# Kernel tuning notes

Hardware: AMD Instinct MI355X
Metric: run time of the kernel (lower is better)

Reference implementation:

```python
import jax, jax.numpy as jnp
import numpy as np

N_NODES = 100000
N_EDGES = 1600000
HIDDEN = 128
NUM_FILTERS = 128
NUM_GAUSSIANS = 50
CUTOFF = 10.0
BOX = 5.0  # positions in [0,5]^3 so all pairwise distances < cutoff


def shifted_softplus(x):
    return jax.nn.softplus(x) - jnp.log(2.0)


def setup_inputs() -> dict:
    key = jax.random.key(0)
    ks = jax.random.split(key, 12)
    h = jax.random.normal(ks[0], (N_NODES, HIDDEN), jnp.float32)
    pos = jax.random.uniform(ks[1], (N_NODES, 3), jnp.float32) * BOX
    edge_index = jax.random.randint(ks[2], (2, N_EDGES), 0, N_NODES, jnp.int32)
    def lin(k, fan_in, fan_out):
        s = 1.0 / np.sqrt(fan_in)
        return jax.random.uniform(k, (fan_in, fan_out), jnp.float32, -s, s)
    return {
        "h": h,
        "pos": pos,
        "edge_index": edge_index,
        # CFConv filter network: Linear(NG, NF) -> ssp -> Linear(NF, NF)
        "mlp_w1": lin(ks[3], NUM_GAUSSIANS, NUM_FILTERS),
        "mlp_b1": jnp.zeros((NUM_FILTERS,), jnp.float32),
        "mlp_w2": lin(ks[4], NUM_FILTERS, NUM_FILTERS),
        "mlp_b2": jnp.zeros((NUM_FILTERS,), jnp.float32),
        # CFConv lin1 (no bias), lin2
        "lin1_w": lin(ks[5], HIDDEN, NUM_FILTERS),
        "lin2_w": lin(ks[6], NUM_FILTERS, HIDDEN),
        "lin2_b": jnp.zeros((HIDDEN,), jnp.float32),
        # InteractionBlock output linear
        "lin_w": lin(ks[7], HIDDEN, HIDDEN),
        "lin_b": jnp.zeros((HIDDEN,), jnp.float32),
    }


def reference(h, pos, edge_index, mlp_w1, mlp_b1, mlp_w2, mlp_b2,
              lin1_w, lin2_w, lin2_b, lin_w, lin_b):
    row, col = edge_index[0], edge_index[1]
    # edge distances (radius_graph neighbor list precomputed in setup_inputs)
    d = jnp.linalg.norm(pos[row] - pos[col], axis=-1)  # [E]
    # Gaussian smearing
    offset = jnp.linspace(0.0, CUTOFF, NUM_GAUSSIANS)
    coeff = -0.5 / (offset[1] - offset[0]) ** 2
    edge_attr = jnp.exp(coeff * (d[:, None] - offset[None, :]) ** 2)  # [E, NG]
    # CFConv: cosine cutoff * filter MLP
    C = 0.5 * (jnp.cos(d * jnp.pi / CUTOFF) + 1.0)  # [E]
    W = shifted_softplus(edge_attr @ mlp_w1 + mlp_b1) @ mlp_w2 + mlp_b2
    W = W * C[:, None]  # [E, NF]
    x = h @ lin1_w  # [N, NF]
    msgs = x[col] * W  # gather source feats, modulate by filter
    agg = jax.ops.segment_sum(msgs, row, num_segments=h.shape[0])  # scatter-add
    x = agg @ lin2_w + lin2_b
    # InteractionBlock tail: act -> linear
    x = shifted_softplus(x)
    x = x @ lin_w + lin_b
    return x
```

## Files before the change

### kernel.cpp

```cpp
#include <hip/hip_runtime.h>
#include <hip/hip_fp16.h>
#include <math.h>

constexpr int N_NODES = 100000;
constexpr int N_EDGES = 1600000;
constexpr int H       = 128;
constexpr int NG      = 50;
constexpr int EPT     = 32;
constexpr int NT      = N_EDGES / EPT;
constexpr int EBLK    = 2560;
constexpr int NBINS   = 98 * 1024;
constexpr int NODEB   = N_NODES / 32;

typedef _Float16 f16x8 __attribute__((ext_vector_type(8)));
typedef float    f32x4 __attribute__((ext_vector_type(4)));

__device__ __forceinline__ float ssp_fast(float v) {
    return fmaxf(v, 0.0f) + __logf(1.0f + __expf(-fabsf(v))) - 0.69314718056f;
}

__device__ __forceinline__ void stage_tile_fp16(
    const float* __restrict__ src, _Float16* lds, int tid)
{
    const int row = tid >> 3;
    const int c0  = (tid & 7) * 16;
    const float* s = src + row * H + c0;
    #pragma unroll
    for (int half = 0; half < 2; ++half) {
        float4 f0 = *reinterpret_cast<const float4*>(s + half * 8);
        float4 f1 = *reinterpret_cast<const float4*>(s + half * 8 + 4);
        f16x8 v;
        v[0] = (_Float16)f0.x; v[1] = (_Float16)f0.y;
        v[2] = (_Float16)f0.z; v[3] = (_Float16)f0.w;
        v[4] = (_Float16)f1.x; v[5] = (_Float16)f1.y;
        v[6] = (_Float16)f1.z; v[7] = (_Float16)f1.w;
        unsigned off = (unsigned)(row * H + c0 + half * 8) * 2u;
        off ^= (unsigned)((row & 7) << 4);
        *reinterpret_cast<f16x8*>(reinterpret_cast<char*>(lds) + off) = v;
    }
}

__global__ __launch_bounds__(256) void prep0_kernel(
    const float* __restrict__ h, const float* __restrict__ w,
    __half* __restrict__ x, int* __restrict__ bins, float* __restrict__ agg)
{
    __shared__ alignas(16) _Float16 a_lds[32 * H];

    const int tid  = threadIdx.x;
    const int gtid = blockIdx.x * 256 + tid;
    const int gsz  = NODEB * 256;

    for (int i = gtid; i < NBINS; i += gsz) bins[i] = 0;
    {
        float4 z = {0.0f, 0.0f, 0.0f, 0.0f};
        float4* agg4 = reinterpret_cast<float4*>(agg);
        for (int i = gtid; i < N_NODES * H / 4; i += gsz) agg4[i] = z;
    }

    const int wv  = tid >> 6;
    const int l   = tid & 63;
    const int lhi = l >> 4;
    const int llo = l & 15;

    f16x8 bf[2][4];
    #pragma unroll
    for (int nf = 0; nf < 2; ++nf) {
        const int n = wv * 32 + nf * 16 + llo;
        #pragma unroll
        for (int ks = 0; ks < 4; ++ks)
            #pragma unroll
            for (int i = 0; i < 8; ++i)
                bf[nf][ks][i] = (_Float16)w[(ks * 32 + lhi * 8 + i) * H + n];
    }

    stage_tile_fp16(h + (size_t)blockIdx.x * 32 * H, a_lds, tid);
    __syncthreads();

    const f32x4 zero4 = {0.0f, 0.0f, 0.0f, 0.0f};
    f32x4 c[2][2];
    #pragma unroll
    for (int m = 0; m < 2; ++m)
        #pragma unroll
        for (int nf = 0; nf < 2; ++nf) c[m][nf] = zero4;

    #pragma unroll
    for (int msub = 0; msub < 2; ++msub) {
        const int rowa = msub * 16 + llo;
        #pragma unroll
        for (int ks = 0; ks < 4; ++ks) {
            unsigned off = (unsigned)(rowa * H) * 2u + (unsigned)(ks * 64 + lhi * 16);
            off ^= (unsigned)((rowa & 7) << 4);
            const f16x8 a = *reinterpret_cast<const f16x8*>(
                reinterpret_cast<const char*>(a_lds) + off);
            #pragma unroll
            for (int nf = 0; nf < 2; ++nf)
                c[msub][nf] = __builtin_amdgcn_mfma_f32_16x16x32_f16(
                    a, bf[nf][ks], c[msub][nf], 0, 0, 0);
        }
    }

    #pragma unroll
    for (int msub = 0; msub < 2; ++msub)
        #pragma unroll
        for (int nf = 0; nf < 2; ++nf)
            #pragma unroll
            for (int j = 0; j < 4; ++j) {
                const int node = blockIdx.x * 32 + msub * 16 + lhi * 4 + j;
                const int filt = wv * 32 + nf * 16 + llo;
                x[(size_t)node * H + filt] = __float2half(c[msub][nf][j]);
            }
}

__global__ __launch_bounds__(256) void hist_kernel(
    const int* __restrict__ ei, int* __restrict__ bins)
{
    const int e = blockIdx.x * 256 + threadIdx.x;
    if (e < N_EDGES) atomicAdd(&bins[ei[e]], 1);
}

__global__ __launch_bounds__(1024) void scanA_kernel(
    int* __restrict__ bins, int* __restrict__ bsum)
{
    __shared__ int ts[1024];
    const int i = blockIdx.x * 1024 + threadIdx.x;
    const int v = bins[i];
    ts[threadIdx.x] = v;
    __syncthreads();
    for (int d = 1; d < 1024; d <<= 1) {
        int t = (threadIdx.x >= d) ? ts[threadIdx.x - d] : 0;
        __syncthreads();
        ts[threadIdx.x] += t;
        __syncthreads();
    }
    bins[i] = ts[threadIdx.x] - v;
    if (threadIdx.x == 1023) bsum[blockIdx.x] = ts[1023];
}

__global__ __launch_bounds__(128) void scanB_kernel(int* __restrict__ bsum)
{
    __shared__ int ts[128];
    const int i = threadIdx.x;
    const int v = (i < 98) ? bsum[i] : 0;
    ts[i] = v;
    __syncthreads();
    for (int d = 1; d < 128; d <<= 1) {
        int t = (i >= d) ? ts[i - d] : 0;
        __syncthreads();
        ts[i] += t;
        __syncthreads();
    }
    if (i < 98) bsum[i] = ts[i] - v;
}

__global__ __launch_bounds__(256) void scatter_kernel(
    const int* __restrict__ ei, int* __restrict__ bins,
    const int* __restrict__ bsum, int2* __restrict__ srt)
{
    const int e = blockIdx.x * 256 + threadIdx.x;
    if (e < N_EDGES) {
        const int r = ei[e];
        const int c = ei[N_EDGES + e];
        const int p = atomicAdd(&bins[r], 1) + bsum[r >> 10];
        srt[p] = make_int2(r, c);
    }
}

__global__ __launch_bounds__(256) void edge_kernel(
    const float* __restrict__ pos, const int2* __restrict__ srt,
    const __half* __restrict__ x,
    const float* __restrict__ w1, const float* __restrict__ b1,
    const float* __restrict__ w2, const float* __restrict__ b2,
    float* __restrict__ agg)
{
    __shared__ alignas(16) _Float16 t_lds[EPT * H];
    __shared__ alignas(16) _Float16 attr_lds[EPT * 64];

    const int tid = threadIdx.x;
    const int w   = tid >> 6;
    const int l   = tid & 63;
    const int lhi = l >> 4;
    const int llo = l & 15;

    constexpr float GSTEP = 10.0f / 49.0f;
    constexpr float GCOEF = -12.005f;
    constexpr float PIC   = 0.31415926535897931f;

    f16x8 b1f[2][2];
    #pragma unroll
    for (int nf = 0; nf < 2; ++nf) {
        const int n = w * 32 + nf * 16 + llo;
        #pragma unroll
        for (int ks = 0; ks < 2; ++ks) {
            #pragma unroll
            for (int i = 0; i < 8; ++i) {
                const int k = ks * 32 + lhi * 8 + i;
                b1f[nf][ks][i] = (k < NG) ? (_Float16)w1[k * H + n] : (_Float16)0.0f;
            }
        }
    }
    f16x8 b2f[2][4];
    #pragma unroll
    for (int nf = 0; nf < 2; ++nf) {
        const int n = w * 32 + nf * 16 + llo;
        #pragma unroll
        for (int ks = 0; ks < 4; ++ks) {
            #pragma unroll
            for (int i = 0; i < 8; ++i) {
                const int k = ks * 32 + lhi * 8 + i;
                b2f[nf][ks][i] = (_Float16)w2[k * H + n];
            }
        }
    }
    const float b1v[2] = { b1[w * 32 + llo], b1[w * 32 + 16 + llo] };
    const float b2v[2] = { b2[w * 32 + llo], b2[w * 32 + 16 + llo] };

    const f32x4 zero4 = {0.0f, 0.0f, 0.0f, 0.0f};

    int rC = 0, cC = 0; float dC = 0.0f, ccC = 0.0f;
    auto load_edge = [&](int t, int& r, int& c, float& d, float& cc) {
        const int2 rc = srt[t * EPT + (l & 31)];
        r = rc.x;
        c = rc.y;
        const float dx = pos[3 * r + 0] - pos[3 * c + 0];
        const float dy = pos[3 * r + 1] - pos[3 * c + 1];
        const float dz = pos[3 * r + 2] - pos[3 * c + 2];
        d  = sqrtf(dx * dx + dy * dy + dz * dz);
        cc = 0.5f * cosf(d * PIC) + 0.5f;
    };
    if (l < 32) load_edge(blockIdx.x, rC, cC, dC, ccC);

    for (int t = blockIdx.x; t < NT; t += gridDim.x) {
        {
            const int ae = w * 8 + (l >> 3);
            const int g0 = (l & 7) * 8;
            const float de = __shfl(dC, ae);
            f16x8 av;
            #pragma unroll
            for (int i = 0; i < 8; ++i) {
                const float diff = de - (float)(g0 + i) * GSTEP;
                av[i] = (_Float16)__expf(GCOEF * diff * diff);
            }
            unsigned off = (unsigned)(ae * 128 + (l & 7) * 16);
            off ^= (unsigned)((ae & 7) << 4);
            *reinterpret_cast<f16x8*>(
                reinterpret_cast<char*>(attr_lds) + off) = av;
        }

        int rN = 0, cN = 0; float dN = 0.0f, ccN = 0.0f;
        const int tn = t + gridDim.x;
        if (l < 32 && tn < NT) load_edge(tn, rN, cN, dN, ccN);

        __syncthreads();

        float xv[2][4][2];
        #pragma unroll
        for (int msub = 0; msub < 2; ++msub)
            #pragma unroll
            for (int j = 0; j < 4; ++j) {
                const int edge  = msub * 16 + lhi * 4 + j;
                const int ce    = __shfl(cC, edge);
                const int cbase = ce * H + w * 32 + llo;
                xv[msub][j][0] = __half2float(x[cbase]);
                xv[msub][j][1] = __half2float(x[cbase + 16]);
            }

        f32x4 c1[2][2];
        #pragma unroll
        for (int m = 0; m < 2; ++m)
            #pragma unroll
            for (int nf = 0; nf < 2; ++nf) c1[m][nf] = zero4;

        #pragma unroll
        for (int msub = 0; msub < 2; ++msub) {
            const int ea = msub * 16 + llo;
            #pragma unroll
            for (int ks = 0; ks < 2; ++ks) {
                unsigned off = (unsigned)(ea * 128 + ks * 64 + lhi * 16);
                off ^= (unsigned)((ea & 7) << 4);
                const f16x8 a1 = *reinterpret_cast<const f16x8*>(
                    reinterpret_cast<const char*>(attr_lds) + off);
                #pragma unroll
                for (int nf = 0; nf < 2; ++nf)
                    c1[msub][nf] = __builtin_amdgcn_mfma_f32_16x16x32_f16(
                        a1, b1f[nf][ks], c1[msub][nf], 0, 0, 0);
            }
        }

        #pragma unroll
        for (int msub = 0; msub < 2; ++msub)
            #pragma unroll
            for (int nf = 0; nf < 2; ++nf)
                #pragma unroll
                for (int j = 0; j < 4; ++j) {
                    const int edge = msub * 16 + lhi * 4 + j;
                    const int filt = w * 32 + nf * 16 + llo;
                    const float tv = ssp_fast(c1[msub][nf][j] + b1v[nf]);
                    unsigned off = (unsigned)(edge * H + filt) * 2u;
                    off ^= (unsigned)((edge & 7) << 4);
                    *reinterpret_cast<_Float16*>(
                        reinterpret_cast<char*>(t_lds) + off) = (_Float16)tv;
                }

        __syncthreads();

        f32x4 c2[2][2];
        #pragma unroll
        for (int m = 0; m < 2; ++m)
            #pragma unroll
            for (int nf = 0; nf < 2; ++nf) c2[m][nf] = zero4;

        #pragma unroll
        for (int ks = 0; ks < 4; ++ks) {
            f16x8 a2[2];
            #pragma unroll
            for (int msub = 0; msub < 2; ++msub) {
                const int edge = msub * 16 + llo;
                unsigned off = (unsigned)(edge * H) * 2u
                             + (unsigned)(ks * 64 + lhi * 16);
                off ^= (unsigned)((edge & 7) << 4);
                a2[msub] = *reinterpret_cast<const f16x8*>(
                    reinterpret_cast<const char*>(t_lds) + off);
            }
            #pragma unroll
            for (int msub = 0; msub < 2; ++msub)
                #pragma unroll
                for (int nf = 0; nf < 2; ++nf)
                    c2[msub][nf] = __builtin_amdgcn_mfma_f32_16x16x32_f16(
                        a2[msub], b2f[nf][ks], c2[msub][nf], 0, 0, 0);
        }

        #pragma unroll
        for (int msub = 0; msub < 2; ++msub) {
            int rr[4]; float cce[4];
            #pragma unroll
            for (int j = 0; j < 4; ++j) {
                const int edge = msub * 16 + lhi * 4 + j;
                rr[j]  = __shfl(rC, edge);
                cce[j] = __shfl(ccC, edge);
            }
            const bool bB1 = rr[1] != rr[0];
            const bool bB2 = rr[2] != rr[1];
            const bool bB3 = rr[3] != rr[2];
            const bool closed = bB1 | bB2 | bB3;
            const int  prev_t = __shfl_up(rr[3], 16);
            const int  next_h = __shfl_down(rr[0], 16);
            const bool mrg  = (lhi > 0) && (rr[0] == prev_t);
            const bool sing = !closed;
            const bool issue_tail = (lhi == 3) || (next_h != rr[3]);

            float v0[4], v1[4];
            #pragma unroll
            for (int j = 0; j < 4; ++j) {
                v0[j] = (c2[msub][0][j] + b2v[0]) * cce[j] * xv[msub][j][0];
                v1[j] = (c2[msub][1][j] + b2v[1]) * cce[j] * xv[msub][j][1];
            }
            const int fc0 = w * 32 + llo;
            const int fc1 = fc0 + 16;

            float h0 = v0[0], h1 = v1[0];
            if (!bB1) { h0 += v0[1]; h1 += v1[1];
                if (!bB2) { h0 += v0[2]; h1 += v1[2];
                    if (!bB3) { h0 += v0[3]; h1 += v1[3]; } } }
            float cs0 = v0[3], cs1 = v1[3];
            if (!bB3) { cs0 += v0[2]; cs1 += v1[2];
                if (!bB2) { cs0 += v0[1]; cs1 += v1[1];
                    if (!bB1) { cs0 += v0[0]; cs1 += v1[0]; } } }

            if (bB1 && bB2) { atomicAdd(&agg[rr[1] * H + fc0], v0[1]);
                              atomicAdd(&agg[rr[1] * H + fc1], v1[1]); }
            if (bB2 && bB3) { atomicAdd(&agg[rr[2] * H + fc0], v0[2]);
                              atomicAdd(&agg[rr[2] * H + fc1], v1[2]); }
            if (bB1 && !bB2 && bB3) {
                atomicAdd(&agg[rr[1] * H + fc0], v0[1] + v0[2]);
                atomicAdd(&agg[rr[1] * H + fc1], v1[1] + v1[2]);
            }

            bool f = !(sing && mrg);
            {
                float p0 = __shfl_up(cs0, 16), p1 = __shfl_up(cs1, 16);
                int   pf = __shfl_up((int)f, 16);
                if (lhi >= 1 && !f) { cs0 += p0; cs1 += p1; f = (bool)pf; }
            }
            {
                float p0 = __shfl_up(cs0, 32), p1 = __shfl_up(cs1, 32);
                int   pf = __shfl_up((int)f, 32);
                if (lhi >= 2 && !f) { cs0 += p0; cs1 += p1; f = (bool)pf; }
            }
            const float car0 = __shfl_up(cs0, 16);
            const float car1 = __shfl_up(cs1, 16);

            if (closed) {
                atomicAdd(&agg[rr[0] * H + fc0], h0 + (mrg ? car0 : 0.0f));
                atomicAdd(&agg[rr[0] * H + fc1], h1 + (mrg ? car1 : 0.0f));
            }
            if (issue_tail) {
                atomicAdd(&agg[rr[3] * H + fc0], cs0);
                atomicAdd(&agg[rr[3] * H + fc1], cs1);
            }
        }

        rC = rN; cC = cN; dC = dN; ccC = ccN;
    }
}

__global__ __launch_bounds__(256) void final_kernel(
    const float* __restrict__ agg,
    const float* __restrict__ w2l, const float* __restrict__ b2l,
    const float* __restrict__ wl,  const float* __restrict__ bl,
    float* __restrict__ out)
{
    __shared__ alignas(16) _Float16 a_lds[32 * H];
    __shared__ alignas(16) _Float16 t_lds[32 * H];

    const int tid = threadIdx.x;
    const int wv  = tid >> 6;
    const int l   = tid & 63;
    const int lhi = l >> 4;
    const int llo = l & 15;

    f16x8 b1f[2][4], b2f[2][4];
    #pragma unroll
    for (int nf = 0; nf < 2; ++nf) {
        const int n = wv * 32 + nf * 16 + llo;
        #pragma unroll
        for (int ks = 0; ks < 4; ++ks)
            #pragma unroll
            for (int i = 0; i < 8; ++i) {
                const int k = ks * 32 + lhi * 8 + i;
                b1f[nf][ks][i] = (_Float16)w2l[k * H + n];
                b2f[nf][ks][i] = (_Float16)wl[k * H + n];
            }
    }
    const float b2v[2] = { b2l[wv * 32 + llo], b2l[wv * 32 + 16 + llo] };
    const float bv[2]  = { bl[wv * 32 + llo],  bl[wv * 32 + 16 + llo]  };

    stage_tile_fp16(agg + (size_t)blockIdx.x * 32 * H, a_lds, tid);
    __syncthreads();

    const f32x4 zero4 = {0.0f, 0.0f, 0.0f, 0.0f};
    f32x4 c1[2][2];
    #pragma unroll
    for (int m = 0; m < 2; ++m)
        #pragma unroll
        for (int nf = 0; nf < 2; ++nf) c1[m][nf] = zero4;

    #pragma unroll
    for (int msub = 0; msub < 2; ++msub) {
        const int rowa = msub * 16 + llo;
        #pragma unroll
        for (int ks = 0; ks < 4; ++ks) {
            unsigned off = (unsigned)(rowa * H) * 2u + (unsigned)(ks * 64 + lhi * 16);
            off ^= (unsigned)((rowa & 7) << 4);
            const f16x8 a = *reinterpret_cast<const f16x8*>(
                reinterpret_cast<const char*>(a_lds) + off);
            #pragma unroll
            for (int nf = 0; nf < 2; ++nf)
                c1[msub][nf] = __builtin_amdgcn_mfma_f32_16x16x32_f16(
                    a, b1f[nf][ks], c1[msub][nf], 0, 0, 0);
        }
    }

    #pragma unroll
    for (int msub = 0; msub < 2; ++msub)
        #pragma unroll
        for (int nf = 0; nf < 2; ++nf)
            #pragma unroll
            for (int j = 0; j < 4; ++j) {
                const int rowc = msub * 16 + lhi * 4 + j;
                const int filt = wv * 32 + nf * 16 + llo;
                const float tv = ssp_fast(c1[msub][nf][j] + b2v[nf]);
                unsigned off = (unsigned)(rowc * H + filt) * 2u;
                off ^= (unsigned)((rowc & 7) << 4);
                *reinterpret_cast<_Float16*>(
                    reinterpret_cast<char*>(t_lds) + off) = (_Float16)tv;
            }

    __syncthreads();

    f32x4 c2[2][2];
    #pragma unroll
    for (int m = 0; m < 2; ++m)
        #pragma unroll
        for (int nf = 0; nf < 2; ++nf) c2[m][nf] = zero4;

    #pragma unroll
    for (int msub = 0; msub < 2; ++msub) {
        const int rowa = msub * 16 + llo;
        #pragma unroll
        for (int ks = 0; ks < 4; ++ks) {
            unsigned off = (unsigned)(rowa * H) * 2u + (unsigned)(ks * 64 + lhi * 16);
            off ^= (unsigned)((rowa & 7) << 4);
            const f16x8 a = *reinterpret_cast<const f16x8*>(
                reinterpret_cast<const char*>(t_lds) + off);
            #pragma unroll
            for (int nf = 0; nf < 2; ++nf)
                c2[msub][nf] = __builtin_amdgcn_mfma_f32_16x16x32_f16(
                    a, b2f[nf][ks], c2[msub][nf], 0, 0, 0);
        }
    }

    #pragma unroll
    for (int msub = 0; msub < 2; ++msub)
        #pragma unroll
        for (int nf = 0; nf < 2; ++nf)
            #pragma unroll
            for (int j = 0; j < 4; ++j) {
                const int node = blockIdx.x * 32 + msub * 16 + lhi * 4 + j;
                const int filt = wv * 32 + nf * 16 + llo;
                out[(size_t)node * H + filt] = c2[msub][nf][j] + bv[nf];
            }
}

extern "C" void kernel_launch(void* const* d_in, const int* in_sizes, int n_in,
                              void* d_out, int out_size, void* d_ws, size_t ws_size,
                              hipStream_t stream) {
    const float* h      = (const float*)d_in[0];
    const float* pos    = (const float*)d_in[1];
    const int*   ei     = (const int*)  d_in[2];
    const float* mlp_w1 = (const float*)d_in[3];
    const float* mlp_b1 = (const float*)d_in[4];
    const float* mlp_w2 = (const float*)d_in[5];
    const float* mlp_b2 = (const float*)d_in[6];
    const float* lin1_w = (const float*)d_in[7];
    const float* lin2_w = (const float*)d_in[8];
    const float* lin2_b = (const float*)d_in[9];
    const float* lin_w  = (const float*)d_in[10];
    const float* lin_b  = (const float*)d_in[11];

    float* out = (float*)d_out;
    char*  ws  = (char*)d_ws;
    float* agg  = (float*)ws;
    char*  p    = ws + (size_t)N_NODES * H * 4;
    int*   bins = (int*)p;
    int*   bsum = (int*)(p + (size_t)NBINS * 4);
    int2*  srt  = (int2*)(p + (size_t)NBINS * 4 + 512);
    __half* x   = (__half*)d_out;

    prep0_kernel<<<NODEB, 256, 0, stream>>>(h, lin1_w, x, bins, agg);
    hist_kernel<<<(N_EDGES + 255) / 256, 256, 0, stream>>>(ei, bins);
    scanA_kernel<<<NBINS / 1024, 1024, 0, stream>>>(bins, bsum);
    scanB_kernel<<<1, 128, 0, stream>>>(bsum);
    scatter_kernel<<<(N_EDGES + 255) / 256, 256, 0, stream>>>(ei, bins, bsum, srt);

    edge_kernel<<<EBLK, 256, 0, stream>>>(pos, srt, x, mlp_w1, mlp_b1,
                                          mlp_w2, mlp_b2, agg);
    final_kernel<<<NODEB, 256, 0, stream>>>(agg, lin2_w, lin2_b,
                                            lin_w, lin_b, out);
}
```

Before: 576.8 us.

## Precompute edge distance and cutoff in scatter; sparse Gaussian smearing in edge kernel

The small bsum scan is folded into every scatter block, which removes one launch. Edge distance and cosine cutoff are now computed in the scatter pass and stored with the sorted (row, col) as an int4 record. The edge kernel then reads this record directly instead of gathering pos and shuffling across lanes. Gaussian smearing now evaluates only a 16-wide window of Gaussians around each distance and zero-fills the rest. This cuts exp work, at the cost of an extra LDS clear plus barrier per tile and a small approximation from the truncated tails. The sorted metadata doubles in size and is stored in the output buffer's spare space.

```diff
diff --git a/kernel.cpp b/kernel.cpp
--- a/kernel.cpp
+++ b/kernel.cpp
@@ -13,6 +13,7 @@
 constexpr int NODEB   = N_NODES / 32;
 
 typedef _Float16 f16x8 __attribute__((ext_vector_type(8)));
+typedef _Float16 f16x2 __attribute__((ext_vector_type(2)));
 typedef float    f32x4 __attribute__((ext_vector_type(4)));
 
 __device__ __forceinline__ float ssp_fast(float v) {
@@ -136,38 +137,44 @@
     if (threadIdx.x == 1023) bsum[blockIdx.x] = ts[1023];
 }
 
-__global__ __launch_bounds__(128) void scanB_kernel(int* __restrict__ bsum)
-{
-    __shared__ int ts[128];
-    const int i = threadIdx.x;
-    const int v = (i < 98) ? bsum[i] : 0;
-    ts[i] = v;
+__global__ __launch_bounds__(256) void scatter_kernel(
+    const int* __restrict__ ei, const float* __restrict__ pos,
+    int* __restrict__ bins, const int* __restrict__ bsum,
+    int4* __restrict__ meta)
+{
+    __shared__ int pre[128];
+    const int tid = threadIdx.x;
+    int myv = 0;
+    if (tid < 128) {
+        myv = (tid < 98) ? bsum[tid] : 0;
+        pre[tid] = myv;
+    }
     __syncthreads();
     for (int d = 1; d < 128; d <<= 1) {
-        int t = (i >= d) ? ts[i - d] : 0;
-        __syncthreads();
-        ts[i] += t;
-        __syncthreads();
-    }
-    if (i < 98) bsum[i] = ts[i] - v;
-}
-
-__global__ __launch_bounds__(256) void scatter_kernel(
-    const int* __restrict__ ei, int* __restrict__ bins,
-    const int* __restrict__ bsum, int2* __restrict__ srt)
-{
-    const int e = blockIdx.x * 256 + threadIdx.x;
+        int t = (tid < 128 && tid >= d) ? pre[tid - d] : 0;
+        __syncthreads();
+        if (tid < 128) pre[tid] += t;
+        __syncthreads();
+    }
+    if (tid < 128) pre[tid] -= myv;
+    __syncthreads();
+
+    const int e = blockIdx.x * 256 + tid;
     if (e < N_EDGES) {
         const int r = ei[e];
         const int c = ei[N_EDGES + e];
-        const int p = atomicAdd(&bins[r], 1) + bsum[r >> 10];
-        srt[p] = make_int2(r, c);
+        const int p = atomicAdd(&bins[r], 1) + pre[r >> 10];
+        const float dx = pos[3 * r + 0] - pos[3 * c + 0];
+        const float dy = pos[3 * r + 1] - pos[3 * c + 1];
+        const float dz = pos[3 * r + 2] - pos[3 * c + 2];
+        const float d  = sqrtf(dx * dx + dy * dy + dz * dz);
+        const float cc = 0.5f * cosf(d * 0.31415926535897931f) + 0.5f;
+        meta[p] = make_int4(r, __float_as_int(cc), c, __float_as_int(d));
     }
 }
 
 __global__ __launch_bounds__(256) void edge_kernel(
-    const float* __restrict__ pos, const int2* __restrict__ srt,
-    const __half* __restrict__ x,
+    const int4* __restrict__ meta, const __half* __restrict__ x,
     const float* __restrict__ w1, const float* __restrict__ b1,
     const float* __restrict__ w2, const float* __restrict__ b2,
     float* __restrict__ agg)
@@ -182,8 +189,8 @@
     const int llo = l & 15;
 
     constexpr float GSTEP = 10.0f / 49.0f;
+    constexpr float GINV  = 4.9f;
     constexpr float GCOEF = -12.005f;
-    constexpr float PIC   = 0.31415926535897931f;
 
     f16x8 b1f[2][2];
     #pragma unroll
@@ -215,41 +222,35 @@
     const float b2v[2] = { b2[w * 32 + llo], b2[w * 32 + 16 + llo] };
 
     const f32x4 zero4 = {0.0f, 0.0f, 0.0f, 0.0f};
-
-    int rC = 0, cC = 0; float dC = 0.0f, ccC = 0.0f;
-    auto load_edge = [&](int t, int& r, int& c, float& d, float& cc) {
-        const int2 rc = srt[t * EPT + (l & 31)];
-        r = rc.x;
-        c = rc.y;
-        const float dx = pos[3 * r + 0] - pos[3 * c + 0];
-        const float dy = pos[3 * r + 1] - pos[3 * c + 1];
-        const float dz = pos[3 * r + 2] - pos[3 * c + 2];
-        d  = sqrtf(dx * dx + dy * dy + dz * dz);
-        cc = 0.5f * cosf(d * PIC) + 0.5f;
-    };
-    if (l < 32) load_edge(blockIdx.x, rC, cC, dC, ccC);
+    const f16x8 zf16  = {(_Float16)0, (_Float16)0, (_Float16)0, (_Float16)0,
+                         (_Float16)0, (_Float16)0, (_Float16)0, (_Float16)0};
 
     for (int t = blockIdx.x; t < NT; t += gridDim.x) {
+        const int4* mt = meta + (size_t)t * EPT;
+
+        *reinterpret_cast<f16x8*>(
+            reinterpret_cast<char*>(attr_lds) + tid * 16) = zf16;
+        __syncthreads();
+
         {
-            const int ae = w * 8 + (l >> 3);
-            const int g0 = (l & 7) * 8;
-            const float de = __shfl(dC, ae);
-            f16x8 av;
-            #pragma unroll
-            for (int i = 0; i < 8; ++i) {
-                const float diff = de - (float)(g0 + i) * GSTEP;
-                av[i] = (_Float16)__expf(GCOEF * diff * diff);
-            }
-            unsigned off = (unsigned)(ae * 128 + (l & 7) * 16);
+            const int ae = tid >> 3;
+            const int p  = tid & 7;
+            const float d = __int_as_float(
+                reinterpret_cast<const int*>(mt + ae)[3]);
+            int g0 = (int)(d * GINV + 0.5f) - 7;
+            g0 &= ~1;
+            g0 = max(0, min(48, g0));
+            const int g = g0 + 2 * p;
+            const float df0 = d - (float)g * GSTEP;
+            const float df1 = d - (float)(g + 1) * GSTEP;
+            f16x2 v;
+            v[0] = (_Float16)__expf(GCOEF * df0 * df0);
+            v[1] = (_Float16)__expf(GCOEF * df1 * df1);
+            unsigned off = (unsigned)(ae * 128 + g * 2);
             off ^= (unsigned)((ae & 7) << 4);
-            *reinterpret_cast<f16x8*>(
-                reinterpret_cast<char*>(attr_lds) + off) = av;
-        }
-
-        int rN = 0, cN = 0; float dN = 0.0f, ccN = 0.0f;
-        const int tn = t + gridDim.x;
-        if (l < 32 && tn < NT) load_edge(tn, rN, cN, dN, ccN);
-
+            *reinterpret_cast<f16x2*>(
+                reinterpret_cast<char*>(attr_lds) + off) = v;
+        }
         __syncthreads();
 
         float xv[2][4][2];
@@ -257,9 +258,9 @@
         for (int msub = 0; msub < 2; ++msub)
             #pragma unroll
             for (int j = 0; j < 4; ++j) {
-                const int edge  = msub * 16 + lhi * 4 + j;
-                const int ce    = __shfl(cC, edge);
-                const int cbase = ce * H + w * 32 + llo;
+                const int edge = msub * 16 + lhi * 4 + j;
+                const int col  = reinterpret_cast<const int*>(mt + edge)[2];
+                const int cbase = col * H + w * 32 + llo;
                 xv[msub][j][0] = __half2float(x[cbase]);
                 xv[msub][j][1] = __half2float(x[cbase + 16]);
             }
@@ -303,6 +304,14 @@
 
         __syncthreads();
 
+        int2 rcA[2][4];
+        #pragma unroll
+        for (int msub = 0; msub < 2; ++msub)
+            #pragma unroll
+            for (int j = 0; j < 4; ++j)
+                rcA[msub][j] = *reinterpret_cast<const int2*>(
+                    mt + msub * 16 + lhi * 4 + j);
+
         f32x4 c2[2][2];
         #pragma unroll
         for (int m = 0; m < 2; ++m)
@@ -334,9 +343,8 @@
             int rr[4]; float cce[4];
             #pragma unroll
             for (int j = 0; j < 4; ++j) {
-                const int edge = msub * 16 + lhi * 4 + j;
-                rr[j]  = __shfl(rC, edge);
-                cce[j] = __shfl(ccC, edge);
+                rr[j]  = rcA[msub][j].x;
+                cce[j] = __int_as_float(rcA[msub][j].y);
             }
             const bool bB1 = rr[1] != rr[0];
             const bool bB2 = rr[2] != rr[1];
@@ -398,8 +406,6 @@
                 atomicAdd(&agg[rr[3] * H + fc1], cs1);
             }
         }
-
-        rC = rN; cC = cN; dC = dN; ccC = ccN;
     }
 }
 
@@ -533,16 +539,16 @@
     char*  p    = ws + (size_t)N_NODES * H * 4;
     int*   bins = (int*)p;
     int*   bsum = (int*)(p + (size_t)NBINS * 4);
-    int2*  srt  = (int2*)(p + (size_t)NBINS * 4 + 512);
-    __half* x   = (__half*)d_out;
+
+    __half* x    = (__half*)d_out;
+    int4*   meta = (int4*)((char*)d_out + (size_t)N_NODES * H * 2);
 
     prep0_kernel<<<NODEB, 256, 0, stream>>>(h, lin1_w, x, bins, agg);
     hist_kernel<<<(N_EDGES + 255) / 256, 256, 0, stream>>>(ei, bins);
     scanA_kernel<<<NBINS / 1024, 1024, 0, stream>>>(bins, bsum);
-    scanB_kernel<<<1, 128, 0, stream>>>(bsum);
-    scatter_kernel<<<(N_EDGES + 255) / 256, 256, 0, stream>>>(ei, bins, bsum, srt);
-
-    edge_kernel<<<EBLK, 256, 0, stream>>>(pos, srt, x, mlp_w1, mlp_b1,
+    scatter_kernel<<<(N_EDGES + 255) / 256, 256, 0, stream>>>(ei, pos, bins,
+                                                              bsum, meta);
+    edge_kernel<<<EBLK, 256, 0, stream>>>(meta, x, mlp_w1, mlp_b1,
                                           mlp_w2, mlp_b2, agg);
     final_kernel<<<NODEB, 256, 0, stream>>>(agg, lin2_w, lin2_b,
                                             lin_w, lin_b, out);
```

Measured after the change: 501.8 us. -13.0%, faster.
